# Kernel tuning notes

Hardware: AMD Instinct MI355X
Metric: run time of the kernel (lower is better)

## Reference

```python
import jax, jax.numpy as jnp
import numpy as np
import math

B, S, D, H = 64, 512, 768, 12
HS = D // H  # head size = 64


def setup_inputs() -> dict:
    key = jax.random.key(0)
    ks = jax.random.split(key, 8)
    scale = 1.0 / math.sqrt(D)
    return {
        "from_tensor": jax.random.normal(ks[0], (B, S, D), jnp.float32),
        "to_tensor": jax.random.normal(ks[1], (B, S, D), jnp.float32),
        "Wq": jax.random.normal(ks[2], (D, D), jnp.float32) * scale,
        "bq": jax.random.normal(ks[3], (D,), jnp.float32) * 0.02,
        "Wk": jax.random.normal(ks[4], (D, D), jnp.float32) * scale,
        "bk": jax.random.normal(ks[5], (D,), jnp.float32) * 0.02,
        "Wv": jax.random.normal(ks[6], (D, D), jnp.float32) * scale,
        "bv": jax.random.normal(ks[7], (D,), jnp.float32) * 0.02,
    }


def _split_heads(x):
    # [B, S, D] -> [B, H, S, HS]
    return x.reshape(B, S, H, HS).transpose(0, 2, 1, 3)


def reference(from_tensor, to_tensor, Wq, bq, Wk, bk, Wv, bv):
    q = _split_heads(from_tensor @ Wq + bq)
    k = _split_heads(to_tensor @ Wk + bk)
    v = _split_heads(to_tensor @ Wv + bv)
    scores = jnp.einsum("bhqd,bhkd->bhqk", q, k) / math.sqrt(HS)
    probs = jax.nn.softmax(scores, axis=-1)
    out = jnp.einsum("bhqk,bhkd->bhqd", probs, v)
    return out.transpose(0, 2, 1, 3).reshape(B, S, D)
```

## Files before the change

kernel.cpp:

```cpp
#include <hip/hip_runtime.h>
#include <hip/hip_bf16.h>

#define GAS __attribute__((address_space(1)))
#define LAS __attribute__((address_space(3)))

typedef __attribute__((ext_vector_type(8))) short   bf16x8;
typedef __attribute__((ext_vector_type(4))) float   f32x4;
typedef __attribute__((ext_vector_type(4))) float   f4;
typedef __attribute__((ext_vector_type(8))) short   s8v;
typedef __attribute__((ext_vector_type(2))) unsigned int u32x2;

#define NB  64
#define NS  512
#define ND  768
#define NH  12
#define NHS 64
#define NM  (NB*NS)
#define NBH (NB*NH)

#define QSCALE 0.18033688011112042f

__device__ __forceinline__ unsigned short f2bf(float x){
  unsigned int u = __float_as_uint(x);
  u += 0x7fffu + ((u >> 16) & 1u);
  return (unsigned short)(u >> 16);
}

__device__ __forceinline__ f32x4 mfma16(bf16x8 a, bf16x8 b, f32x4 c){
  return __builtin_amdgcn_mfma_f32_16x16x32_bf16(a, b, c, 0, 0, 0);
}

__global__ void cvt_x(const float* __restrict__ from_t, const float* __restrict__ to_t,
                      short* __restrict__ fb, short* __restrict__ tb){
  int v = blockIdx.x * 256 + threadIdx.x;
  const int NG = NM * ND / 8;
  const float* s; short* d;
  if (v < NG){ s = from_t; d = fb; } else { s = to_t; d = tb; v -= NG; }
  f4 a = ((const f4*)s)[(long)v * 2];
  f4 b = ((const f4*)s)[(long)v * 2 + 1];
  s8v o;
  o[0]=(short)f2bf(a[0]); o[1]=(short)f2bf(a[1]); o[2]=(short)f2bf(a[2]); o[3]=(short)f2bf(a[3]);
  o[4]=(short)f2bf(b[0]); o[5]=(short)f2bf(b[1]); o[6]=(short)f2bf(b[2]); o[7]=(short)f2bf(b[3]);
  ((s8v*)d)[v] = o;
}

__global__ void cvt_w(const float* __restrict__ Wq, const float* __restrict__ Wk,
                      const float* __restrict__ Wv, short* __restrict__ Wt){
  int i = blockIdx.x * 256 + threadIdx.x;
  int mat = i / (ND*ND);
  int rem = i - mat * (ND*ND);
  int k = rem / ND;
  int n = rem - k * ND;
  const float* W = (mat == 0) ? Wq : (mat == 1 ? Wk : Wv);
  Wt[(long)mat*ND*ND + (long)n*ND + k] = (short)f2bf(W[rem]);
}

__global__ __launch_bounds__(512, 2)
void qkv_gemm(const short* __restrict__ Xf, const short* __restrict__ Xt,
              const short* __restrict__ Wt,
              const float* __restrict__ bq, const float* __restrict__ bk,
              const float* __restrict__ bv,
              short* __restrict__ Qw, short* __restrict__ Kw, short* __restrict__ Vtw){
  __shared__ short smem[49152];

  int bid = blockIdx.x;
  int wg  = (bid & 7) * 144 + (bid >> 3);
  int mat = wg / 384;
  int r   = wg - mat * 384;
  int mt  = r / 3;
  int nt  = r - mt * 3;

  const short* A  = (mat == 0) ? Xf : Xt;
  const short* Wp = Wt + (long)mat * ND * ND;

  int t_ = threadIdx.x, wv = t_ >> 6, l = t_ & 63, g = l >> 4, c = l & 15;
  int wm = wv >> 2, wn = wv & 3;
  int m0 = mt * 256, n0 = nt * 256;

  short* As[3] = { smem, smem + 8192, smem + 16384 };
  short* Bs[3] = { smem + 24576, smem + 32768, smem + 40960 };

  auto stage = [&](int kt, short* Ab, short* Bb, int ci){
    int chunk = ci * 8 + wv;
    int ch = chunk & 15;
    int idx = ch * 64 + l;
    int row = idx >> 2, slot = idx & 3;
    int kcol = kt * 32 + ((slot ^ ((row >> 1) & 3)) << 3);
    if (chunk < 16){
      const short* gp = A + (long)(m0 + row) * ND + kcol;
      __builtin_amdgcn_global_load_lds((const GAS unsigned int*)gp,
                                       (LAS unsigned int*)(Ab + ch * 512), 16, 0, 0);
    } else {
      const short* gp = Wp + (long)(n0 + row) * ND + kcol;
      __builtin_amdgcn_global_load_lds((const GAS unsigned int*)gp,
                                       (LAS unsigned int*)(Bb + ch * 512), 16, 0, 0);
    }
  };

  f32x4 zero = {0.f, 0.f, 0.f, 0.f};
  f32x4 acc[8][4];
  #pragma unroll
  for (int i = 0; i < 8; ++i)
    #pragma unroll
    for (int j = 0; j < 4; ++j) acc[i][j] = zero;

  #pragma unroll
  for (int ci = 0; ci < 4; ++ci) stage(0, As[0], Bs[0], ci);
  #pragma unroll
  for (int ci = 0; ci < 4; ++ci) stage(1, As[1], Bs[1], ci);

  auto step = [&](const short* Asl, const short* Bsl, short* An, short* Bn, int t){
    if (t == 23) asm volatile("s_waitcnt vmcnt(0)" ::: "memory");
    else         asm volatile("s_waitcnt vmcnt(4)" ::: "memory");
    __builtin_amdgcn_s_barrier();
    bf16x8 af[8], bfr[4];
    #pragma unroll
    for (int ms = 0; ms < 4; ++ms){
      int row = wm * 128 + ms * 16 + c;
      af[ms] = *(const bf16x8*)(Asl + row * 32 + ((g ^ ((row >> 1) & 3)) << 3));
    }
    if (t < 22) stage(t + 2, An, Bn, 0);
    #pragma unroll
    for (int ns = 0; ns < 4; ++ns){
      int row = wn * 64 + ns * 16 + c;
      bfr[ns] = *(const bf16x8*)(Bsl + row * 32 + ((g ^ ((row >> 1) & 3)) << 3));
    }
    if (t < 22) stage(t + 2, An, Bn, 1);
    #pragma unroll
    for (int ms = 4; ms < 8; ++ms){
      int row = wm * 128 + ms * 16 + c;
      af[ms] = *(const bf16x8*)(Asl + row * 32 + ((g ^ ((row >> 1) & 3)) << 3));
    }
    if (t < 22){ stage(t + 2, An, Bn, 2); stage(t + 2, An, Bn, 3); }
    __builtin_amdgcn_s_setprio(1);
    #pragma unroll
    for (int ms = 0; ms < 8; ++ms)
      #pragma unroll
      for (int ns = 0; ns < 4; ++ns)
        acc[ms][ns] = mfma16(af[ms], bfr[ns], acc[ms][ns]);
    __builtin_amdgcn_s_setprio(0);
  };

  for (int it = 0; it < 8; ++it){
    int t = it * 3;
    step(As[0], Bs[0], As[2], Bs[2], t);
    step(As[1], Bs[1], As[0], Bs[0], t + 1);
    step(As[2], Bs[2], As[1], Bs[1], t + 2);
  }

  __builtin_amdgcn_s_barrier();

  int n0g = n0 + wn * 64;
  const float* bias = (mat == 0) ? bq : (mat == 1 ? bk : bv);
  float bb[4];
  #pragma unroll
  for (int ns = 0; ns < 4; ++ns) bb[ns] = bias[n0g + ns * 16 + c];
  short* chunk = smem + wv * 4096;
  int hq = n0g >> 6;

  if (mat < 2){
    short* O = (mat == 0) ? Qw : Kw;
    float scl = (mat == 0) ? QSCALE : 1.0f;
    #pragma unroll
    for (int sp = 0; sp < 2; ++sp){
      #pragma unroll
      for (int msl = 0; msl < 4; ++msl){
        #pragma unroll
        for (int ns = 0; ns < 4; ++ns){
          int col = ns * 16 + c;
          #pragma unroll
          for (int i = 0; i < 4; ++i){
            int row = msl * 16 + g * 4 + i;
            chunk[row * 64 + (((col >> 3) ^ (row & 7)) << 3) + (col & 7)] =
                (short)f2bf((acc[sp * 4 + msl][ns][i] + bb[ns]) * scl);
          }
        }
      }
      asm volatile("s_waitcnt lgkmcnt(0)" ::: "memory");
      __builtin_amdgcn_sched_barrier(0);
      #pragma unroll
      for (int rr = 0; rr < 8; ++rr){
        int row = rr * 8 + (l >> 3);
        int slot = l & 7;
        bf16x8 v = *(const bf16x8*)(chunk + row * 64 + ((slot ^ (row & 7)) << 3));
        int m = m0 + wm * 128 + sp * 64 + row;
        int b = m >> 9, s2 = m & 511;
        *(bf16x8*)(O + (((long)(b * NH + hq) * NS + s2) << 6) + slot * 8) = v;
      }
      if (sp == 0){ asm volatile("s_waitcnt lgkmcnt(0)" ::: "memory"); }
    }
  } else {
    #pragma unroll
    for (int sp = 0; sp < 2; ++sp){
      #pragma unroll
      for (int msl = 0; msl < 4; ++msl){
        #pragma unroll
        for (int ns = 0; ns < 4; ++ns){
          int hs = ns * 16 + c;
          #pragma unroll
          for (int i = 0; i < 4; ++i){
            int col = msl * 16 + g * 4 + i;
            chunk[hs * 64 + (((col >> 3) ^ (hs & 7)) << 3) + (col & 7)] =
                (short)f2bf(acc[sp * 4 + msl][ns][i] + bb[ns]);
          }
        }
      }
      asm volatile("s_waitcnt lgkmcnt(0)" ::: "memory");
      __builtin_amdgcn_sched_barrier(0);
      int mbase = m0 + wm * 128 + sp * 64;
      int b = mbase >> 9, s0 = mbase & 511;
      #pragma unroll
      for (int rr = 0; rr < 8; ++rr){
        int hs = rr * 8 + (l >> 3);
        int slot = l & 7;
        bf16x8 v = *(const bf16x8*)(chunk + hs * 64 + ((slot ^ (hs & 7)) << 3));
        *(bf16x8*)(Vtw + (long)((b * NH + hq) * 64 + hs) * NS + s0 + slot * 8) = v;
      }
      if (sp == 0){ asm volatile("s_waitcnt lgkmcnt(0)" ::: "memory"); }
    }
  }
}

__global__ __launch_bounds__(512, 1)
void attn_kernel(const short* __restrict__ Qw, const short* __restrict__ Kw,
                 const short* __restrict__ Vtw, float* __restrict__ out){
  extern __shared__ char smem[];
  short* Ks = (short*)smem;
  short* Vs = (short*)(smem + 65536);
  short* Ps = (short*)(smem + 131072);

  int bh = blockIdx.x;
  int t = threadIdx.x, wv = t >> 6, l = t & 63, g = l >> 4, c = l & 15;

  const short* Kb = Kw  + (long)bh * NS * NHS;
  const short* Vb = Vtw + (long)bh * NS * NHS;

  #pragma unroll
  for (int it = 0; it < 8; ++it){
    int chunk = it * 8 + wv;
    {
      int idx = chunk * 64 + l;
      int row = idx >> 3, slot = idx & 7;
      const short* gk = Kb + row * 64 + ((slot ^ (row & 7)) * 8);
      __builtin_amdgcn_global_load_lds((const GAS unsigned int*)gk,
                                       (LAS unsigned int*)(Ks + chunk * 512), 16, 0, 0);
    }
    {
      int row = chunk, slot = l;
      const short* gv = Vb + (long)row * NS + (((slot & 56) | ((slot & 7) ^ (row & 7))) * 8);
      __builtin_amdgcn_global_load_lds((const GAS unsigned int*)gv,
                                       (LAS unsigned int*)(Vs + chunk * 512), 16, 0, 0);
    }
  }
  __syncthreads();

  short* Pw = Ps + wv * 1024;
  int b = bh / NH, h = bh - b * NH;
  float* outb = out + (long)b * NS * ND + (long)h * 64;

  f32x4 zero = {0.f, 0.f, 0.f, 0.f};

  for (int qg = 0; qg < 4; ++qg){
    int q0 = wv * 64 + qg * 16;
    const short* Qb = Qw + ((long)bh * NS + q0 + c) * 64;
    bf16x8 aq0 = *(const bf16x8*)(Qb + g * 8);
    bf16x8 aq1 = *(const bf16x8*)(Qb + 32 + g * 8);

    f32x4 sc[32];
    #pragma unroll
    for (int j = 0; j < 32; ++j) sc[j] = zero;

    #pragma unroll
    for (int j = 0; j < 32; ++j){
      int key = j * 16 + c;
      const char* base = (const char*)Ks + key * 128;
      bf16x8 b0 = *(const bf16x8*)(base + (((0 + g) ^ (key & 7)) << 4));
      bf16x8 b1 = *(const bf16x8*)(base + (((4 + g) ^ (key & 7)) << 4));
      sc[j] = mfma16(aq0, b0, sc[j]);
      sc[j] = mfma16(aq1, b1, sc[j]);
    }

    float inv[4];
    #pragma unroll
    for (int i = 0; i < 4; ++i){
      float m = sc[0][i];
      #pragma unroll
      for (int j = 1; j < 32; ++j) m = fmaxf(m, sc[j][i]);
      m = fmaxf(m, __shfl_xor(m, 1));
      m = fmaxf(m, __shfl_xor(m, 2));
      m = fmaxf(m, __shfl_xor(m, 4));
      m = fmaxf(m, __shfl_xor(m, 8));
      float s_ = 0.f;
      #pragma unroll
      for (int j = 0; j < 32; ++j){
        float p = exp2f(sc[j][i] - m);
        sc[j][i] = p;
        s_ += p;
      }
      s_ += __shfl_xor(s_, 1);
      s_ += __shfl_xor(s_, 2);
      s_ += __shfl_xor(s_, 4);
      s_ += __shfl_xor(s_, 8);
      inv[i] = 1.f / s_;
    }

    f32x4 o[4];
    #pragma unroll
    for (int ns = 0; ns < 4; ++ns) o[ns] = zero;

    #pragma unroll
    for (int ch = 0; ch < 8; ++ch){
      #pragma unroll
      for (int jl = 0; jl < 4; ++jl){
        int kl = jl * 16 + c;
        int slot = kl >> 3;
        #pragma unroll
        for (int i = 0; i < 4; ++i){
          int q = g * 4 + i;
          int byte = q * 128 + ((slot ^ (q & 7)) << 4) + ((kl & 7) << 1);
          *(short*)((char*)Pw + byte) = (short)f2bf(sc[ch * 4 + jl][i]);
        }
      }
      #pragma unroll
      for (int kk = 0; kk < 2; ++kk){
        int slotp = kk * 4 + g;
        bf16x8 ap = *(const bf16x8*)((const char*)Pw + c * 128 + ((slotp ^ (c & 7)) << 4));
        #pragma unroll
        for (int ns = 0; ns < 4; ++ns){
          int d = ns * 16 + c;
          int slotv = ch * 8 + kk * 4 + g;
          bf16x8 bv8 = *(const bf16x8*)((const char*)Vs + d * 1024 +
                                        (((slotv & 56) | ((slotv & 7) ^ (d & 7))) << 4));
          o[ns] = mfma16(ap, bv8, o[ns]);
        }
      }
    }

    #pragma unroll
    for (int ns = 0; ns < 4; ++ns)
      #pragma unroll
      for (int i = 0; i < 4; ++i){
        int q = q0 + g * 4 + i;
        outb[(long)q * ND + ns * 16 + c] = o[ns][i] * inv[i];
      }
  }
}

extern "C" void kernel_launch(void* const* d_in, const int* in_sizes, int n_in,
                              void* d_out, int out_size, void* d_ws, size_t ws_size,
                              hipStream_t stream){
  const float* from_t = (const float*)d_in[0];
  const float* to_t   = (const float*)d_in[1];
  const float* Wq = (const float*)d_in[2];
  const float* bq = (const float*)d_in[3];
  const float* Wk = (const float*)d_in[4];
  const float* bk = (const float*)d_in[5];
  const float* Wv = (const float*)d_in[6];
  const float* bv = (const float*)d_in[7];

  short* fb  = (short*)d_ws;
  short* tb  = fb  + 25165824;
  short* Wt  = tb  + 25165824;
  short* Qw  = Wt  + 1769472;
  short* Kw  = Qw  + 25165824;
  short* Vtw = Kw  + 25165824;

  cvt_x<<<24576, 256, 0, stream>>>(from_t, to_t, fb, tb);
  cvt_w<<<6912, 256, 0, stream>>>(Wq, Wk, Wv, Wt);
  qkv_gemm<<<1152, 512, 0, stream>>>(fb, tb, Wt, bq, bk, bv, Qw, Kw, Vtw);
  attn_kernel<<<768, 512, 147456, stream>>>(Qw, Kw, Vtw, (float*)d_out);
}
```

Baseline: 350.7 us.

## Rewrite attention inner loop with 32x32 MFMA, online softmax, register-resident P

The attention kernel moves from 16x16x32 MFMA with a full 512-wide score buffer to 32x32x16 MFMA over 32-key chunks, using an online softmax that only rescales when the running max grows by more than a threshold. Probabilities are packed to bf16 in registers and exchanged across half-waves with shuffles instead of round-tripping through LDS. This removes the P shared-memory buffer and its scalar stores, and computes S transposed so output rows are written as float4 vectors. The cost is extra shuffle and conditional-rescale logic, and the lazy-rescale threshold lets exponentials grow up to 2^8 before correction.

```diff
diff --git a/kernel.cpp b/kernel.cpp
--- a/kernel.cpp
+++ b/kernel.cpp
@@ -6,9 +6,11 @@
 
 typedef __attribute__((ext_vector_type(8))) short   bf16x8;
 typedef __attribute__((ext_vector_type(4))) float   f32x4;
+typedef __attribute__((ext_vector_type(16))) float  f32x16;
 typedef __attribute__((ext_vector_type(4))) float   f4;
 typedef __attribute__((ext_vector_type(8))) short   s8v;
 typedef __attribute__((ext_vector_type(2))) unsigned int u32x2;
+typedef __attribute__((ext_vector_type(4))) unsigned int u32x4;
 
 #define NB  64
 #define NS  512
@@ -28,6 +30,20 @@
 
 __device__ __forceinline__ f32x4 mfma16(bf16x8 a, bf16x8 b, f32x4 c){
   return __builtin_amdgcn_mfma_f32_16x16x32_bf16(a, b, c, 0, 0, 0);
+}
+
+__device__ __forceinline__ f32x16 mfma32(bf16x8 a, bf16x8 b, f32x16 c){
+  return __builtin_amdgcn_mfma_f32_32x32x16_bf16(a, b, c, 0, 0, 0);
+}
+
+__device__ __forceinline__ unsigned int cvtpk(float lo, float hi){
+  unsigned int r;
+  asm("v_cvt_pk_bf16_f32 %0, %1, %2" : "=v"(r) : "v"(lo), "v"(hi));
+  return r;
+}
+
+__device__ __forceinline__ bf16x8 u2b(u32x4 u){
+  union { u32x4 a; bf16x8 b; } c; c.a = u; return c.b;
 }
 
 __global__ void cvt_x(const float* __restrict__ from_t, const float* __restrict__ to_t,
@@ -227,10 +243,11 @@
   extern __shared__ char smem[];
   short* Ks = (short*)smem;
   short* Vs = (short*)(smem + 65536);
-  short* Ps = (short*)(smem + 131072);
 
   int bh = blockIdx.x;
-  int t = threadIdx.x, wv = t >> 6, l = t & 63, g = l >> 4, c = l & 15;
+  int t = threadIdx.x, wv = t >> 6, l = t & 63;
+  int lam = l & 31, hi = l >> 5;
+  int r7 = lam & 7;
 
   const short* Kb = Kw  + (long)bh * NS * NHS;
   const short* Vb = Vtw + (long)bh * NS * NHS;
@@ -254,95 +271,104 @@
   }
   __syncthreads();
 
-  short* Pw = Ps + wv * 1024;
   int b = bh / NH, h = bh - b * NH;
   float* outb = out + (long)b * NS * ND + (long)h * 64;
 
-  f32x4 zero = {0.f, 0.f, 0.f, 0.f};
-
-  for (int qg = 0; qg < 4; ++qg){
-    int q0 = wv * 64 + qg * 16;
-    const short* Qb = Qw + ((long)bh * NS + q0 + c) * 64;
-    bf16x8 aq0 = *(const bf16x8*)(Qb + g * 8);
-    bf16x8 aq1 = *(const bf16x8*)(Qb + 32 + g * 8);
-
-    f32x4 sc[32];
-    #pragma unroll
-    for (int j = 0; j < 32; ++j) sc[j] = zero;
-
-    #pragma unroll
-    for (int j = 0; j < 32; ++j){
-      int key = j * 16 + c;
-      const char* base = (const char*)Ks + key * 128;
-      bf16x8 b0 = *(const bf16x8*)(base + (((0 + g) ^ (key & 7)) << 4));
-      bf16x8 b1 = *(const bf16x8*)(base + (((4 + g) ^ (key & 7)) << 4));
-      sc[j] = mfma16(aq0, b0, sc[j]);
-      sc[j] = mfma16(aq1, b1, sc[j]);
-    }
-
-    float inv[4];
-    #pragma unroll
-    for (int i = 0; i < 4; ++i){
-      float m = sc[0][i];
-      #pragma unroll
-      for (int j = 1; j < 32; ++j) m = fmaxf(m, sc[j][i]);
-      m = fmaxf(m, __shfl_xor(m, 1));
-      m = fmaxf(m, __shfl_xor(m, 2));
-      m = fmaxf(m, __shfl_xor(m, 4));
-      m = fmaxf(m, __shfl_xor(m, 8));
-      float s_ = 0.f;
-      #pragma unroll
-      for (int j = 0; j < 32; ++j){
-        float p = exp2f(sc[j][i] - m);
-        sc[j][i] = p;
-        s_ += p;
-      }
-      s_ += __shfl_xor(s_, 1);
-      s_ += __shfl_xor(s_, 2);
-      s_ += __shfl_xor(s_, 4);
-      s_ += __shfl_xor(s_, 8);
-      inv[i] = 1.f / s_;
-    }
-
-    f32x4 o[4];
-    #pragma unroll
-    for (int ns = 0; ns < 4; ++ns) o[ns] = zero;
-
-    #pragma unroll
-    for (int ch = 0; ch < 8; ++ch){
-      #pragma unroll
-      for (int jl = 0; jl < 4; ++jl){
-        int kl = jl * 16 + c;
-        int slot = kl >> 3;
+  for (int qt = 0; qt < 2; ++qt){
+    int q0 = wv * 64 + qt * 32;
+    const short* Qb = Qw + (((long)bh * NS + q0 + lam) << 6) + hi * 8;
+    bf16x8 qf[4];
+    #pragma unroll
+    for (int dk = 0; dk < 4; ++dk) qf[dk] = *(const bf16x8*)(Qb + dk * 16);
+
+    f32x16 o0, o1;
+    #pragma unroll
+    for (int j = 0; j < 16; ++j){ o0[j] = 0.f; o1[j] = 0.f; }
+    float m_run = -1e30f, lsum = 0.f;
+
+    #pragma unroll
+    for (int ch = 0; ch < 16; ++ch){
+      f32x16 s;
+      #pragma unroll
+      for (int j = 0; j < 16; ++j) s[j] = 0.f;
+      const char* kbase = (const char*)Ks + (ch * 32 + lam) * 128;
+      #pragma unroll
+      for (int dk = 0; dk < 4; ++dk){
+        bf16x8 kf = *(const bf16x8*)(kbase + (((hi + 2 * dk) ^ r7) << 4));
+        s = mfma32(kf, qf[dk], s);
+      }
+
+      float t8[8], t4[4];
+      #pragma unroll
+      for (int j = 0; j < 8; ++j) t8[j] = fmaxf(s[j], s[j + 8]);
+      #pragma unroll
+      for (int j = 0; j < 4; ++j) t4[j] = fmaxf(t8[j], t8[j + 4]);
+      float m1 = fmaxf(fmaxf(t4[0], t4[1]), fmaxf(t4[2], t4[3]));
+      float pmax = fmaxf(m1, __shfl_xor(m1, 32));
+      if (__any(pmax > m_run + 8.0f)){
+        float mnew = fmaxf(m_run, pmax);
+        float cf = exp2f(m_run - mnew);
+        lsum *= cf;
         #pragma unroll
-        for (int i = 0; i < 4; ++i){
-          int q = g * 4 + i;
-          int byte = q * 128 + ((slot ^ (q & 7)) << 4) + ((kl & 7) << 1);
-          *(short*)((char*)Pw + byte) = (short)f2bf(sc[ch * 4 + jl][i]);
-        }
-      }
-      #pragma unroll
-      for (int kk = 0; kk < 2; ++kk){
-        int slotp = kk * 4 + g;
-        bf16x8 ap = *(const bf16x8*)((const char*)Pw + c * 128 + ((slotp ^ (c & 7)) << 4));
-        #pragma unroll
-        for (int ns = 0; ns < 4; ++ns){
-          int d = ns * 16 + c;
-          int slotv = ch * 8 + kk * 4 + g;
-          bf16x8 bv8 = *(const bf16x8*)((const char*)Vs + d * 1024 +
-                                        (((slotv & 56) | ((slotv & 7) ^ (d & 7))) << 4));
-          o[ns] = mfma16(ap, bv8, o[ns]);
-        }
-      }
-    }
-
-    #pragma unroll
-    for (int ns = 0; ns < 4; ++ns)
-      #pragma unroll
-      for (int i = 0; i < 4; ++i){
-        int q = q0 + g * 4 + i;
-        outb[(long)q * ND + ns * 16 + c] = o[ns][i] * inv[i];
-      }
+        for (int j = 0; j < 16; ++j){ o0[j] *= cf; o1[j] *= cf; }
+        m_run = mnew;
+      }
+      float p[16];
+      #pragma unroll
+      for (int j = 0; j < 16; ++j) p[j] = exp2f(s[j] - m_run);
+      float a8[8], a4[4];
+      #pragma unroll
+      for (int j = 0; j < 8; ++j) a8[j] = p[j] + p[j + 8];
+      #pragma unroll
+      for (int j = 0; j < 4; ++j) a4[j] = a8[j] + a8[j + 4];
+      lsum += (a4[0] + a4[1]) + (a4[2] + a4[3]);
+
+      unsigned int w[8];
+      #pragma unroll
+      for (int rr = 0; rr < 8; ++rr) w[rr] = cvtpk(p[2 * rr], p[2 * rr + 1]);
+      unsigned int y0 = (unsigned int)__shfl_xor((int)(hi ? w[0] : w[2]), 32);
+      unsigned int y1 = (unsigned int)__shfl_xor((int)(hi ? w[1] : w[3]), 32);
+      unsigned int y2 = (unsigned int)__shfl_xor((int)(hi ? w[4] : w[6]), 32);
+      unsigned int y3 = (unsigned int)__shfl_xor((int)(hi ? w[5] : w[7]), 32);
+      u32x4 fa, fb;
+      if (hi){
+        fa[0] = y0;   fa[1] = y1;   fa[2] = w[2]; fa[3] = w[3];
+        fb[0] = y2;   fb[1] = y3;   fb[2] = w[6]; fb[3] = w[7];
+      } else {
+        fa[0] = w[0]; fa[1] = w[1]; fa[2] = y0;   fa[3] = y1;
+        fb[0] = w[4]; fb[1] = w[5]; fb[2] = y2;   fb[3] = y3;
+      }
+      bf16x8 pa = u2b(fa), pb = u2b(fb);
+
+      const char* vb0 = (const char*)Vs + lam * 1024;
+      const char* vb1 = (const char*)Vs + (32 + lam) * 1024;
+      int sl0 = ch * 4 + hi, sl1 = ch * 4 + 2 + hi;
+      int sw0 = ((sl0 & 56) | ((sl0 & 7) ^ r7)) << 4;
+      int sw1 = ((sl1 & 56) | ((sl1 & 7) ^ r7)) << 4;
+      bf16x8 v00 = *(const bf16x8*)(vb0 + sw0);
+      bf16x8 v01 = *(const bf16x8*)(vb0 + sw1);
+      bf16x8 v10 = *(const bf16x8*)(vb1 + sw0);
+      bf16x8 v11 = *(const bf16x8*)(vb1 + sw1);
+      o0 = mfma32(v00, pa, o0);
+      o0 = mfma32(v01, pb, o0);
+      o1 = mfma32(v10, pa, o1);
+      o1 = mfma32(v11, pb, o1);
+    }
+
+    float lt = lsum + __shfl_xor(lsum, 32);
+    float invl = 1.0f / lt;
+    float* orow = outb + (long)(q0 + lam) * ND;
+    #pragma unroll
+    for (int r = 0; r < 4; ++r){
+      f4 u0, u1;
+      #pragma unroll
+      for (int jj = 0; jj < 4; ++jj){
+        u0[jj] = o0[4 * r + jj] * invl;
+        u1[jj] = o1[4 * r + jj] * invl;
+      }
+      *(f4*)(orow + 4 * hi + 8 * r)      = u0;
+      *(f4*)(orow + 32 + 4 * hi + 8 * r) = u1;
+    }
   }
 }
 
@@ -368,5 +394,5 @@
   cvt_x<<<24576, 256, 0, stream>>>(from_t, to_t, fb, tb);
   cvt_w<<<6912, 256, 0, stream>>>(Wq, Wk, Wv, Wt);
   qkv_gemm<<<1152, 512, 0, stream>>>(fb, tb, Wt, bq, bk, bv, Qw, Kw, Vtw);
-  attn_kernel<<<768, 512, 147456, stream>>>(Qw, Kw, Vtw, (float*)d_out);
-}
+  attn_kernel<<<768, 512, 131072, stream>>>(Qw, Kw, Vtw, (float*)d_out);
+}
```

Result: faster. 330.9 us (-5.6%).
